# Performance work log

Measured on AMD Instinct MI355X. Metric: run time of the kernel, lower is better.

Reference implementation:

```python
import jax, jax.numpy as jnp
import numpy as np

B, T, TAU = 4, 512, 512
D_MODEL = 1024  # in_dim == out_dim (required: pos embedding dim out_dim feeds pos_proj with in_size=in_dim)
H, D = 16, 64
LN_EPS = 1e-5


def rel_shift(x):
    # x: [B, T, L, H] -> Transformer-XL relative shift
    b, t, l, h = x.shape
    x = jnp.pad(x, ((0, 0), (0, 0), (1, 0), (0, 0)))  # pad j-dim front
    x = x.reshape(b, l + 1, t, h)[:, 1:, :, :]
    return x.reshape(b, t, l, h)


def setup_inputs() -> dict:
    key = jax.random.key(0)
    ks = jax.random.split(key, 7)
    s = 0.02
    return {
        "inputs": jax.random.normal(ks[0], (B, T, D_MODEL), jnp.float32),
        "memory": jax.random.normal(ks[1], (B, TAU, D_MODEL), jnp.float32),
        "w_qkv": jax.random.normal(ks[2], (3 * H * D, D_MODEL), jnp.float32) * s,
        "w_pos": jax.random.normal(ks[3], (H * D, D_MODEL), jnp.float32) * s,
        "w_out": jax.random.normal(ks[4], (D_MODEL, H * D), jnp.float32) * s,
        "uvar": jax.random.normal(ks[5], (H, D), jnp.float32) * s,
        "vvar": jax.random.normal(ks[6], (H, D), jnp.float32) * s,
        "ln_gamma": jnp.ones((D_MODEL,), jnp.float32),
        "ln_beta": jnp.zeros((D_MODEL,), jnp.float32),
    }


def reference(inputs, memory, w_qkv, w_pos, w_out, uvar, vvar, ln_gamma, ln_beta):
    b, t, din = inputs.shape
    tau = memory.shape[1]
    L = tau + t
    h, d = uvar.shape

    x = jnp.concatenate([jax.lax.stop_gradient(memory), inputs], axis=1)  # [B,L,Din]
    # input layernorm
    mu = jnp.mean(x, axis=-1, keepdims=True)
    var = jnp.mean((x - mu) ** 2, axis=-1, keepdims=True)
    x = (x - mu) / jnp.sqrt(var + LN_EPS) * ln_gamma + ln_beta

    qkv = x @ w_qkv.T  # [B,L,3HD]
    q, k, v = jnp.split(qkv, 3, axis=-1)
    q = q[:, -t:].reshape(b, t, h, d)
    k = k.reshape(b, L, h, d)
    v = v.reshape(b, L, h, d)

    # sinusoidal relative position embedding, dim = out_dim (= din here)
    inv_freq = 1.0 / (10000.0 ** (jnp.arange(0, din, 2, dtype=jnp.float32) / din))
    pos = jnp.arange(L - 1, -1, -1, dtype=jnp.float32)
    sin_in = pos[:, None] * inv_freq[None, :]                 # [L, din/2]
    phi = jnp.concatenate([jnp.sin(sin_in), jnp.cos(sin_in)], axis=-1)  # [L, din]
    R = (phi @ w_pos.T).reshape(L, h, d)

    score = jnp.einsum('bihd,bjhd->bijh', q + uvar, k)        # content score
    pos_score = jnp.einsum('bihd,jhd->bijh', q + vvar, R)     # position score
    score = (score + rel_shift(pos_score)) / (d ** 0.5)       # [B,T,L,H]

    # causal mask: query i attends to j <= tau + i
    mask = (jnp.arange(L)[None, :] <= (tau + jnp.arange(t))[:, None]).astype(score.dtype)
    mask = mask[None, :, :, None]
    masked = score * mask + 1e30 * (mask - 1.0)
    w = jax.nn.softmax(masked, axis=2)

    out = jnp.einsum('bijh,bjhd->bihd', w, v).reshape(b, t, h * d)
    return out @ w_out.T
```

## Files before the change

kernel.cpp:

```cpp
#include <hip/hip_runtime.h>
#include <math.h>

#define B_   4
#define T_   512
#define TAU_ 512
#define L_   1024
#define DM_  1024
#define H_   16
#define D_   64

typedef short  s16x8 __attribute__((ext_vector_type(8)));
typedef ushort u16x4 __attribute__((ext_vector_type(4)));
typedef float  f32x4 __attribute__((ext_vector_type(4)));

__device__ __forceinline__ ushort f2bf(float x) {
  uint u = __float_as_uint(x);
  u += 0x7fffu + ((u >> 16) & 1u);
  return (ushort)(u >> 16);
}
__device__ __forceinline__ float bf2f(ushort u) {
  return __uint_as_float(((uint)u) << 16);
}
__device__ __forceinline__ int sw64(int row, int col) {
  return row * 64 + (col ^ ((row & 7) << 3));
}
template <int CTRL>
__device__ __forceinline__ float dppmov(float x) {
  int xi = __float_as_int(x);
  return __int_as_float(
      __builtin_amdgcn_update_dpp(xi, xi, CTRL, 0xF, 0xF, false));
}

__global__ __launch_bounds__(256) void prep_kernel(
    const float* __restrict__ inp, const float* __restrict__ mem,
    const float* __restrict__ gamma, const float* __restrict__ beta,
    ushort* __restrict__ xn, ushort* __restrict__ phi,
    const float* __restrict__ wq, ushort* __restrict__ wqb,
    const float* __restrict__ wp, ushort* __restrict__ wpb,
    const float* __restrict__ wo, ushort* __restrict__ wob) {
  int blk = blockIdx.x;
  int t = threadIdx.x;
  if (blk < 4096) {
    int row = blk;
    int b = row >> 10, l = row & 1023;
    const float* src = (l < TAU_)
        ? mem + ((size_t)b * TAU_ + l) * DM_
        : inp + ((size_t)b * T_ + (l - TAU_)) * DM_;
    float4 v = *(const float4*)(src + t * 4);
    float s  = v.x + v.y + v.z + v.w;
    float s2 = v.x * v.x + v.y * v.y + v.z * v.z + v.w * v.w;
#pragma unroll
    for (int off = 32; off > 0; off >>= 1) {
      s  += __shfl_down(s, off);
      s2 += __shfl_down(s2, off);
    }
    __shared__ float red[8];
    __shared__ float stat[2];
    int wid = t >> 6;
    if ((t & 63) == 0) { red[wid * 2] = s; red[wid * 2 + 1] = s2; }
    __syncthreads();
    if (t == 0) {
      float ts  = red[0] + red[2] + red[4] + red[6];
      float ts2 = red[1] + red[3] + red[5] + red[7];
      float mu  = ts * (1.0f / DM_);
      float var = ts2 * (1.0f / DM_) - mu * mu;
      stat[0] = mu;
      stat[1] = 1.0f / sqrtf(var + 1e-5f);
    }
    __syncthreads();
    float mu = stat[0], rstd = stat[1];
    float4 g  = *(const float4*)(gamma + t * 4);
    float4 be = *(const float4*)(beta  + t * 4);
    u16x4 o;
    o[0] = f2bf((v.x - mu) * rstd * g.x + be.x);
    o[1] = f2bf((v.y - mu) * rstd * g.y + be.y);
    o[2] = f2bf((v.z - mu) * rstd * g.z + be.z);
    o[3] = f2bf((v.w - mu) * rstd * g.w + be.w);
    *(u16x4*)(xn + (size_t)row * DM_ + t * 4) = o;
  } else if (blk < 8192) {
    int idx = (blk - 4096) * 256 + t;
    int m = idx >> 10, c = idx & 1023;
    float p = (float)(1023 - m);
    int cc = (c < 512) ? c : c - 512;
    float invf = __expf(-((float)(2 * cc) * (1.0f / 1024.0f)) * 9.210340371976184f);
    float a = p * invf;
    phi[idx] = f2bf((c < 512) ? sinf(a) : cosf(a));
  } else {
    int i = (blk - 8192) * 256 + t;
    const float* src; ushort* dst; int off;
    if (i < 786432)       { src = wq; dst = wqb; off = i; }
    else if (i < 1048576) { src = wp; dst = wpb; off = i - 786432; }
    else                  { src = wo; dst = wob; off = i - 1048576; }
    float4 v = *(const float4*)(src + (size_t)off * 4);
    u16x4 o = { f2bf(v.x), f2bf(v.y), f2bf(v.z), f2bf(v.w) };
    *(u16x4*)(dst + (size_t)off * 4) = o;
  }
}

template <typename CT>
__device__ __forceinline__ void gemm_nt_body(
    const ushort* __restrict__ A, const ushort* __restrict__ B,
    CT* __restrict__ C, int M, int N, int K, int bx, int by) {
  __shared__ __attribute__((aligned(16))) ushort As[128 * 64];
  __shared__ __attribute__((aligned(16))) ushort Bs[128 * 64];
  int t = threadIdx.x;
  int w = t >> 6, lane = t & 63, g = lane >> 4, low = lane & 15;
  int wr = w >> 1, wc = w & 1;
  int m0 = by * 128, n0 = bx * 128;
  f32x4 acc[4][4] = {};

  for (int kt = 0; kt < K; kt += 64) {
    __syncthreads();
#pragma unroll
    for (int q = 0; q < 4; ++q) {
      int c = t + q * 256;
      int row = c >> 3;
      int gslot = (c & 7) ^ (row & 7);
      const ushort* ga = A + (size_t)(m0 + row) * K + kt + gslot * 8;
      const ushort* gb = B + (size_t)(n0 + row) * K + kt + gslot * 8;
      __builtin_amdgcn_global_load_lds(
          (const __attribute__((address_space(1))) void*)ga,
          (__attribute__((address_space(3))) void*)&As[(q * 256 + w * 64) * 8],
          16, 0, 0);
      __builtin_amdgcn_global_load_lds(
          (const __attribute__((address_space(1))) void*)gb,
          (__attribute__((address_space(3))) void*)&Bs[(q * 256 + w * 64) * 8],
          16, 0, 0);
    }
    __syncthreads();

#pragma unroll
    for (int kc = 0; kc < 2; ++kc) {
      s16x8 af[4], bfr[4];
#pragma unroll
      for (int mi = 0; mi < 4; ++mi) {
        int row = wr * 64 + mi * 16 + low;
        af[mi] = *(const s16x8*)&As[row * 64 + (((4 * kc + g) ^ (row & 7)) * 8)];
      }
#pragma unroll
      for (int ni = 0; ni < 4; ++ni) {
        int col = wc * 64 + ni * 16 + low;
        bfr[ni] = *(const s16x8*)&Bs[col * 64 + (((4 * kc + g) ^ (col & 7)) * 8)];
      }
#pragma unroll
      for (int mi = 0; mi < 4; ++mi)
#pragma unroll
        for (int ni = 0; ni < 4; ++ni)
          acc[mi][ni] = __builtin_amdgcn_mfma_f32_16x16x32_bf16(
              af[mi], bfr[ni], acc[mi][ni], 0, 0, 0);
    }
  }
#pragma unroll
  for (int mi = 0; mi < 4; ++mi)
#pragma unroll
    for (int ni = 0; ni < 4; ++ni)
#pragma unroll
      for (int r = 0; r < 4; ++r) {
        int m = m0 + wr * 64 + mi * 16 + 4 * g + r;
        int n = n0 + wc * 64 + ni * 16 + low;
        if constexpr (sizeof(CT) == 2)
          C[(size_t)m * N + n] = f2bf(acc[mi][ni][r]);
        else
          C[(size_t)m * N + n] = acc[mi][ni][r];
      }
}

__global__ __launch_bounds__(256) void qkv_r_gemm(
    const ushort* __restrict__ xnb, const ushort* __restrict__ wqb,
    ushort* __restrict__ qkvB,
    const ushort* __restrict__ phib, const ushort* __restrict__ wpb,
    ushort* __restrict__ RmB) {
  int orig = blockIdx.x;
  int id = (orig & 7) * 104 + (orig >> 3);
  if (id < 768)
    gemm_nt_body<ushort>(xnb, wqb, qkvB, 4096, 3072, 1024, id % 24, id / 24);
  else {
    id -= 768;
    gemm_nt_body<ushort>(phib, wpb, RmB, 1024, 1024, 1024, id % 8, id / 8);
  }
}

__global__ __launch_bounds__(256) void out_gemm(
    const ushort* __restrict__ attnb, const ushort* __restrict__ wob,
    float* __restrict__ out) {
  int orig = blockIdx.x;
  int id = (orig & 7) * 16 + (orig >> 3);
  gemm_nt_body<float>(attnb, wob, out, 2048, 1024, 1024, id % 8, id / 8);
}

__global__ __launch_bounds__(256) void attn_mfma_kernel(
    const ushort* __restrict__ qkv, const ushort* __restrict__ Rm,
    const float* __restrict__ uvar, const float* __restrict__ vvar,
    ushort* __restrict__ attn) {
  __shared__ __attribute__((aligned(16))) ushort Ks[2][64 * 64];
  __shared__ __attribute__((aligned(16))) ushort Vt[2][64 * 64];
  __shared__ __attribute__((aligned(16))) ushort Rs[2][128 * 64];
  __shared__ __attribute__((aligned(16))) ushort Pp[4][16 * 64];

  int t   = threadIdx.x;
  int w   = t >> 6;
  int lw  = t & 63;
  int g   = lw >> 4;
  int low = lw & 15;

  int bid = blockIdx.x;
  int bi  = bid & 7;
  int h   = (bid >> 3) & 15;
  int b   = bid >> 7;
  int i0  = bi * 64;
  int lb_w = 48 - 16 * w;

  auto stage_kr = [&](int buf, int tl) {
    int j0s = tl * 64;
#pragma unroll
    for (int q = 0; q < 2; ++q) {
      int c = t + q * 256;
      int row = c >> 3;
      int sl = (c & 7) ^ (row & 7);
      const ushort* srck = qkv + (size_t)(b * L_ + j0s + row) * 3072 +
                           1024 + h * 64 + sl * 8;
      __builtin_amdgcn_global_load_lds(
          (const __attribute__((address_space(1))) void*)srck,
          (__attribute__((address_space(3))) void*)&Ks[buf][(q * 256 + w * 64) * 8],
          16, 0, 0);
    }
    int mb = j0s + 448 - i0;
#pragma unroll
    for (int q = 0; q < 4; ++q) {
      int c = t + q * 256;
      int row = c >> 3;
      int m = mb + row; m = (m > 1023) ? 1023 : m;
      int sl = (c & 7) ^ (row & 7);
      const ushort* srcr = Rm + (size_t)m * 1024 + h * 64 + sl * 8;
      __builtin_amdgcn_global_load_lds(
          (const __attribute__((address_space(1))) void*)srcr,
          (__attribute__((address_space(3))) void*)&Rs[buf][(q * 256 + w * 64) * 8],
          16, 0, 0);
    }
  };

  int vj  = t & 63;
  int vd0 = (t >> 6) * 8;
  float4 vreg[2];
  auto vload = [&](int tl) {
    const ushort* p = qkv + (size_t)(b * L_ + tl * 64 + vj) * 3072 + 2048 + h * 64;
    vreg[0] = *(const float4*)(p + vd0);
    vreg[1] = *(const float4*)(p + vd0 + 32);
  };
  auto vwrite = [&](int buf) {
#pragma unroll
    for (int it = 0; it < 2; ++it) {
      ushort vals[8];
      *(float4*)vals = vreg[it];
#pragma unroll
      for (int e = 0; e < 8; ++e) {
        int d = it * 32 + vd0 + e;
        Vt[buf][d * 64 + (vj ^ ((d & 7) << 3))] = vals[e];
      }
    }
  };

  int iq = i0 + 16 * w + low;
  s16x8 qu[2], qv[2];
  {
    const ushort* qrow = qkv + (size_t)(b * L_ + TAU_ + iq) * 3072 + h * 64;
    const float* ur = uvar + h * 64;
    const float* vr = vvar + h * 64;
#pragma unroll
    for (int kc = 0; kc < 2; ++kc) {
      int dbase = kc * 32 + 8 * g;
#pragma unroll
      for (int e = 0; e < 8; ++e) {
        float q = bf2f(qrow[dbase + e]);
        qu[kc][e] = (short)f2bf(q + ur[dbase + e]);
        qv[kc][e] = (short)f2bf(q + vr[dbase + e]);
      }
    }
  }

  f32x4 O[4] = {};
  float mreg[4] = {-INFINITY, -INFINITY, -INFINITY, -INFINITY};
  float lreg[4] = {0.f, 0.f, 0.f, 0.f};

  int ntiles = 9 + bi;
  stage_kr(0, 0);
  vload(0);
  vwrite(0);
  __syncthreads();
  int cur = 0;
  for (int tile = 0; tile < ntiles; ++tile) {
    int j0 = tile * 64;
    bool more = (tile + 1 < ntiles);
    if (more) { stage_kr(cur ^ 1, tile + 1); vload(tile + 1); }

    f32x4 s[4] = {};
#pragma unroll
    for (int jt = 0; jt < 4; ++jt) {
#pragma unroll
      for (int kc = 0; kc < 2; ++kc) {
        s16x8 kb = *(const s16x8*)&Ks[cur][sw64(jt * 16 + low, kc * 32 + 8 * g)];
        s[jt] = __builtin_amdgcn_mfma_f32_16x16x32_bf16(qu[kc], kb, s[jt], 0, 0, 0);
      }
    }
    f32x4 p[5] = {};
#pragma unroll
    for (int mt = 0; mt < 5; ++mt) {
#pragma unroll
      for (int kc = 0; kc < 2; ++kc) {
        s16x8 rb = *(const s16x8*)&Rs[cur][sw64(lb_w + mt * 16 + low, kc * 32 + 8 * g)];
        p[mt] = __builtin_amdgcn_mfma_f32_16x16x32_bf16(qv[kc], rb, p[mt], 0, 0, 0);
      }
    }
#pragma unroll
    for (int r = 0; r < 4; ++r) {
      int iL = 4 * g + r;
      int src = g * 16 + ((low + 15 - iL) & 15);
      float sh0 = __shfl(p[0][r], src);
      float sh1 = __shfl(p[1][r], src);
      float sh2 = __shfl(p[2][r], src);
      float sh3 = __shfl(p[3][r], src);
      float sh4 = __shfl(p[4][r], src);
      bool lo = (low <= iL);
      float po0 = lo ? sh0 : sh1;
      float po1 = lo ? sh1 : sh2;
      float po2 = lo ? sh2 : sh3;
      float po3 = lo ? sh3 : sh4;
      int lim = TAU_ + i0 + 16 * w + iL;
      s[0][r] = (j0 +  0 + low <= lim) ? (s[0][r] + po0) * 0.125f : -1e30f;
      s[1][r] = (j0 + 16 + low <= lim) ? (s[1][r] + po1) * 0.125f : -1e30f;
      s[2][r] = (j0 + 32 + low <= lim) ? (s[2][r] + po2) * 0.125f : -1e30f;
      s[3][r] = (j0 + 48 + low <= lim) ? (s[3][r] + po3) * 0.125f : -1e30f;
    }
#pragma unroll
    for (int r = 0; r < 4; ++r) {
      float mx = fmaxf(fmaxf(s[0][r], s[1][r]), fmaxf(s[2][r], s[3][r]));
      mx = fmaxf(mx, dppmov<0xB1>(mx));
      mx = fmaxf(mx, dppmov<0x4E>(mx));
      mx = fmaxf(mx, dppmov<0x124>(mx));
      mx = fmaxf(mx, dppmov<0x128>(mx));
      float mn = fmaxf(mreg[r], mx);
      float alpha = __expf(mreg[r] - mn);
      mreg[r] = mn;
      float sum = 0.f;
#pragma unroll
      for (int jt = 0; jt < 4; ++jt) {
        float pe = __expf(s[jt][r] - mn);
        s[jt][r] = pe;
        sum += pe;
      }
      sum += dppmov<0xB1>(sum);
      sum += dppmov<0x4E>(sum);
      sum += dppmov<0x124>(sum);
      sum += dppmov<0x128>(sum);
      lreg[r] = lreg[r] * alpha + sum;
      O[0][r] *= alpha; O[1][r] *= alpha; O[2][r] *= alpha; O[3][r] *= alpha;
    }
#pragma unroll
    for (int jt = 0; jt < 4; ++jt)
#pragma unroll
      for (int r = 0; r < 4; ++r)
        Pp[w][sw64(4 * g + r, jt * 16 + low)] = f2bf(s[jt][r]);
    asm volatile("s_waitcnt lgkmcnt(0)" ::: "memory");
    s16x8 pa0 = *(const s16x8*)&Pp[w][sw64(low, 8 * g)];
    s16x8 pa1 = *(const s16x8*)&Pp[w][sw64(low, 32 + 8 * g)];
#pragma unroll
    for (int dt = 0; dt < 4; ++dt) {
      s16x8 v0 = *(const s16x8*)&Vt[cur][sw64(dt * 16 + low, 8 * g)];
      s16x8 v1 = *(const s16x8*)&Vt[cur][sw64(dt * 16 + low, 32 + 8 * g)];
      O[dt] = __builtin_amdgcn_mfma_f32_16x16x32_bf16(pa0, v0, O[dt], 0, 0, 0);
      O[dt] = __builtin_amdgcn_mfma_f32_16x16x32_bf16(pa1, v1, O[dt], 0, 0, 0);
    }
    if (more) vwrite(cur ^ 1);
    __syncthreads();
    cur ^= 1;
  }
  float inv[4];
#pragma unroll
  for (int r = 0; r < 4; ++r) inv[r] = 1.0f / lreg[r];
#pragma unroll
  for (int dt = 0; dt < 4; ++dt)
#pragma unroll
    for (int r = 0; r < 4; ++r)
      attn[((size_t)(b * T_ + i0 + 16 * w + 4 * g + r)) * 1024 +
           h * 64 + dt * 16 + low] = f2bf(O[dt][r] * inv[r]);
}

extern "C" void kernel_launch(void* const* d_in, const int* in_sizes, int n_in,
                              void* d_out, int out_size, void* d_ws, size_t ws_size,
                              hipStream_t stream) {
  const float* inputs = (const float*)d_in[0];
  const float* memory = (const float*)d_in[1];
  const float* w_qkv  = (const float*)d_in[2];
  const float* w_pos  = (const float*)d_in[3];
  const float* w_out  = (const float*)d_in[4];
  const float* uvar   = (const float*)d_in[5];
  const float* vvar   = (const float*)d_in[6];
  const float* gamma  = (const float*)d_in[7];
  const float* beta   = (const float*)d_in[8];
  float* out = (float*)d_out;

  ushort* qkvB = (ushort*)d_ws;
  ushort* xnb  = qkvB + (size_t)4096 * 3072;
  ushort* phib = xnb  + (size_t)4096 * 1024;
  ushort* RmB  = phib + (size_t)1024 * 1024;
  ushort* wqb  = RmB  + (size_t)1024 * 1024;
  ushort* wpb  = wqb  + (size_t)3072 * 1024;
  ushort* wob  = wpb  + (size_t)1024 * 1024;
  ushort* attnb = xnb;

  prep_kernel<<<13312, 256, 0, stream>>>(inputs, memory, gamma, beta, xnb,
                                         phib, w_qkv, wqb, w_pos, wpb, w_out, wob);
  qkv_r_gemm<<<832, 256, 0, stream>>>(xnb, wqb, qkvB, phib, wpb, RmB);
  attn_mfma_kernel<<<dim3(B_ * H_ * 8), 256, 0, stream>>>(qkvB, RmB, uvar, vvar, attnb);
  out_gemm<<<128, 256, 0, stream>>>(attnb, wob, out);
}
```

Before: 211.2 us.

## Use 128x64 tiles for output GEMM, reverse block order, use shfl_xor reductions

The output projection GEMM switches to a 128x64 tile variant and launches 256 blocks instead of 128, so more of the GPU's compute units are occupied. The attention kernel reverses the query-block order for the second half of the batch, aiming to balance causal workload across the dispatch order. The DPP row-reduction helpers are replaced with __shfl_xor butterfly reductions over 16 lanes. The smaller tile lowers data reuse per block, and shfl_xor may be slower than DPP because it goes through LDS-permute hardware.

```diff
diff --git a/kernel.cpp b/kernel.cpp
--- a/kernel.cpp
+++ b/kernel.cpp
@@ -23,12 +23,6 @@
 }
 __device__ __forceinline__ int sw64(int row, int col) {
   return row * 64 + (col ^ ((row & 7) << 3));
-}
-template <int CTRL>
-__device__ __forceinline__ float dppmov(float x) {
-  int xi = __float_as_int(x);
-  return __int_as_float(
-      __builtin_amdgcn_update_dpp(xi, xi, CTRL, 0xF, 0xF, false));
 }
 
 __global__ __launch_bounds__(256) void prep_kernel(
@@ -165,6 +159,80 @@
       }
 }
 
+template <typename CT>
+__device__ __forceinline__ void gemm_nt_body_n64(
+    const ushort* __restrict__ A, const ushort* __restrict__ B,
+    CT* __restrict__ C, int M, int N, int K, int bx, int by) {
+  __shared__ __attribute__((aligned(16))) ushort As[128 * 64];
+  __shared__ __attribute__((aligned(16))) ushort Bs[64 * 64];
+  int t = threadIdx.x;
+  int w = t >> 6, lane = t & 63, g = lane >> 4, low = lane & 15;
+  int wr = w >> 1, wc = w & 1;
+  int m0 = by * 128, n0 = bx * 64;
+  f32x4 acc[4][2] = {};
+
+  for (int kt = 0; kt < K; kt += 64) {
+    __syncthreads();
+#pragma unroll
+    for (int q = 0; q < 4; ++q) {
+      int c = t + q * 256;
+      int row = c >> 3;
+      int gslot = (c & 7) ^ (row & 7);
+      const ushort* ga = A + (size_t)(m0 + row) * K + kt + gslot * 8;
+      __builtin_amdgcn_global_load_lds(
+          (const __attribute__((address_space(1))) void*)ga,
+          (__attribute__((address_space(3))) void*)&As[(q * 256 + w * 64) * 8],
+          16, 0, 0);
+    }
+#pragma unroll
+    for (int q = 0; q < 2; ++q) {
+      int c = t + q * 256;
+      int row = c >> 3;
+      int gslot = (c & 7) ^ (row & 7);
+      const ushort* gb = B + (size_t)(n0 + row) * K + kt + gslot * 8;
+      __builtin_amdgcn_global_load_lds(
+          (const __attribute__((address_space(1))) void*)gb,
+          (__attribute__((address_space(3))) void*)&Bs[(q * 256 + w * 64) * 8],
+          16, 0, 0);
+    }
+    __syncthreads();
+
+#pragma unroll
+    for (int kc = 0; kc < 2; ++kc) {
+      s16x8 af[4], bfr[2];
+#pragma unroll
+      for (int mi = 0; mi < 4; ++mi) {
+        int row = wr * 64 + mi * 16 + low;
+        af[mi] = *(const s16x8*)&As[row * 64 + (((4 * kc + g) ^ (row & 7)) * 8)];
+      }
+#pragma unroll
+      for (int ni = 0; ni < 2; ++ni) {
+        int col = wc * 32 + ni * 16 + low;
+        bfr[ni] = *(const s16x8*)&Bs[col * 64 + (((4 * kc + g) ^ (col & 7)) * 8)];
+      }
+#pragma unroll
+      for (int mi = 0; mi < 4; ++mi)
+#pragma unroll
+        for (int ni = 0; ni < 2; ++ni)
+          acc[mi][ni] = __builtin_amdgcn_mfma_f32_16x16x32_bf16(
+              af[mi], bfr[ni], acc[mi][ni], 0, 0, 0);
+    }
+  }
+#pragma unroll
+  for (int mi = 0; mi < 4; ++mi)
+#pragma unroll
+    for (int ni = 0; ni < 2; ++ni)
+#pragma unroll
+      for (int r = 0; r < 4; ++r) {
+        int m = m0 + wr * 64 + mi * 16 + 4 * g + r;
+        int n = n0 + wc * 32 + ni * 16 + low;
+        if constexpr (sizeof(CT) == 2)
+          C[(size_t)m * N + n] = f2bf(acc[mi][ni][r]);
+        else
+          C[(size_t)m * N + n] = acc[mi][ni][r];
+      }
+}
+
 __global__ __launch_bounds__(256) void qkv_r_gemm(
     const ushort* __restrict__ xnb, const ushort* __restrict__ wqb,
     ushort* __restrict__ qkvB,
@@ -184,8 +252,8 @@
     const ushort* __restrict__ attnb, const ushort* __restrict__ wob,
     float* __restrict__ out) {
   int orig = blockIdx.x;
-  int id = (orig & 7) * 16 + (orig >> 3);
-  gemm_nt_body<float>(attnb, wob, out, 2048, 1024, 1024, id % 8, id / 8);
+  int id = (orig & 7) * 32 + (orig >> 3);
+  gemm_nt_body_n64<float>(attnb, wob, out, 2048, 1024, 1024, id % 16, id / 16);
 }
 
 __global__ __launch_bounds__(256) void attn_mfma_kernel(
@@ -204,9 +272,9 @@
   int low = lw & 15;
 
   int bid = blockIdx.x;
-  int bi  = bid & 7;
   int h   = (bid >> 3) & 15;
   int b   = bid >> 7;
+  int bi  = (b >= 2) ? (7 - (bid & 7)) : (bid & 7);
   int i0  = bi * 64;
   int lb_w = 48 - 16 * w;
 
@@ -334,10 +402,10 @@
 #pragma unroll
     for (int r = 0; r < 4; ++r) {
       float mx = fmaxf(fmaxf(s[0][r], s[1][r]), fmaxf(s[2][r], s[3][r]));
-      mx = fmaxf(mx, dppmov<0xB1>(mx));
-      mx = fmaxf(mx, dppmov<0x4E>(mx));
-      mx = fmaxf(mx, dppmov<0x124>(mx));
-      mx = fmaxf(mx, dppmov<0x128>(mx));
+      mx = fmaxf(mx, __shfl_xor(mx, 1));
+      mx = fmaxf(mx, __shfl_xor(mx, 2));
+      mx = fmaxf(mx, __shfl_xor(mx, 4));
+      mx = fmaxf(mx, __shfl_xor(mx, 8));
       float mn = fmaxf(mreg[r], mx);
       float alpha = __expf(mreg[r] - mn);
       mreg[r] = mn;
@@ -348,10 +416,10 @@
         s[jt][r] = pe;
         sum += pe;
       }
-      sum += dppmov<0xB1>(sum);
-      sum += dppmov<0x4E>(sum);
-      sum += dppmov<0x124>(sum);
-      sum += dppmov<0x128>(sum);
+      sum += __shfl_xor(sum, 1);
+      sum += __shfl_xor(sum, 2);
+      sum += __shfl_xor(sum, 4);
+      sum += __shfl_xor(sum, 8);
       lreg[r] = lreg[r] * alpha + sum;
       O[0][r] *= alpha; O[1][r] *= alpha; O[2][r] *= alpha; O[3][r] *= alpha;
     }
@@ -412,5 +480,5 @@
                                          phib, w_qkv, wqb, w_pos, wpb, w_out, wob);
   qkv_r_gemm<<<832, 256, 0, stream>>>(xnb, wqb, qkvB, phib, wpb, RmB);
   attn_mfma_kernel<<<dim3(B_ * H_ * 8), 256, 0, stream>>>(qkvB, RmB, uvar, vvar, attnb);
-  out_gemm<<<128, 256, 0, stream>>>(attnb, wob, out);
-}
+  out_gemm<<<256, 256, 0, stream>>>(attnb, wob, out);
+}
```

After: 209.1 us. No clear change (-1.0%).
